# Optimization experiments

Hardware: AMD Instinct MI355X
Metric: run time of the kernel (lower is better)

## Reference

```python
import jax, jax.numpy as jnp
import numpy as np

HEADS = 16
DIM_HEAD = 64
SCALE = DIM_HEAD ** -0.5


def setup_inputs() -> dict:
    key = jax.random.key(0)
    k1, k2, k3 = jax.random.split(key, 3)
    B, N, C = 2, 2048, 1024
    inner = HEADS * DIM_HEAD  # 1024
    x = jax.random.normal(k1, (B, N, C), dtype=jnp.float32)
    w_qkv = jax.random.normal(k2, (C, 3 * inner), dtype=jnp.float32) * (C ** -0.5)
    w_proj = jax.random.normal(k3, (inner, C), dtype=jnp.float32) * (inner ** -0.5)
    b_proj = jnp.zeros((C,), dtype=jnp.float32)
    return {"x": x, "w_qkv": w_qkv, "w_proj": w_proj, "b_proj": b_proj}


def reference(x, w_qkv, w_proj, b_proj):
    B, N, C = x.shape
    qkv = x @ w_qkv  # [B, N, 3*inner]
    qkv = qkv.reshape(B, N, 3, HEADS, DIM_HEAD)
    qkv = jnp.transpose(qkv, (2, 0, 3, 1, 4))  # [3, B, H, N, D]
    q, k, v = qkv[0], qkv[1], qkv[2]
    q = q * SCALE
    attn = jnp.einsum('bhnd,bhmd->bhnm', q, k)  # [B, H, N, N]
    attn = jax.nn.softmax(attn, axis=-1)
    out = jnp.einsum('bhnm,bhmd->bhnd', attn, v)  # [B, H, N, D]
    out = jnp.transpose(out, (0, 2, 1, 3)).reshape(B, N, HEADS * DIM_HEAD)
    return out @ w_proj + b_proj
```

## Files before the change

### kernel.cpp

```cpp
#include <hip/hip_runtime.h>
#include <hip/hip_bf16.h>
#include <cstdint>
#include <cstddef>

static constexpr int BATCH = 2;
static constexpr int SEQ   = 2048;
static constexpr int CDIM  = 1024;
static constexpr int ROWS  = BATCH * SEQ;
static constexpr int QKVN  = 3 * CDIM;
static constexpr int QKN   = 2 * CDIM;

typedef short bf16x8 __attribute__((ext_vector_type(8)));
typedef short bf16x4 __attribute__((ext_vector_type(4)));
typedef float f32x4  __attribute__((ext_vector_type(4)));

__device__ inline short f2bf(float f) {
    union { float f; unsigned u; } v; v.f = f;
    unsigned u = v.u;
    u += 0x7fffu + ((u >> 16) & 1u);
    return (short)(u >> 16);
}

__device__ inline unsigned pk_bf16(float a, float b) {
#if __has_builtin(__builtin_amdgcn_cvt_pk_bf16_f32)
    auto r = __builtin_amdgcn_cvt_pk_bf16_f32(a, b);
    return __builtin_bit_cast(unsigned, r);
#else
    union { float f; unsigned u; } ua, ub;
    ua.f = a; ub.f = b;
    unsigned xa = ua.u + 0x7fffu + ((ua.u >> 16) & 1u);
    unsigned xb = ub.u + 0x7fffu + ((ub.u >> 16) & 1u);
    return __builtin_amdgcn_perm(xb, xa, 0x07060302);
#endif
}

__device__ inline void glds16(const short* g, short* l) {
    __builtin_amdgcn_global_load_lds(
        (const __attribute__((address_space(1))) void*)g,
        (__attribute__((address_space(3))) void*)l, 16, 0, 0);
}

__device__ inline f32x4 mfma16_bf16(bf16x4 a, bf16x4 b, f32x4 c) {
#if __has_builtin(__builtin_amdgcn_mfma_f32_16x16x16bf16_1k)
    return __builtin_amdgcn_mfma_f32_16x16x16bf16_1k(a, b, c, 0, 0, 0);
#else
    asm("v_mfma_f32_16x16x16_bf16 %0, %1, %2, %0" : "+v"(c) : "v"(a), "v"(b));
    return c;
#endif
}

__global__ __launch_bounds__(256) void prep(const float* __restrict__ x,
                                            const float* __restrict__ wqkv,
                                            const float* __restrict__ wproj,
                                            short* __restrict__ x_bf,
                                            short* __restrict__ wqkvT,
                                            short* __restrict__ wprojT,
                                            float smul) {
    __shared__ float tile[32][33];
    const int bid = blockIdx.x, t = threadIdx.x;
    if (bid < 4096) {
        int i = bid * 256 + t;
        float4 f = ((const float4*)x)[i];
        uint2 o;
        o.x = pk_bf16(f.x, f.y);
        o.y = pk_bf16(f.z, f.w);
        ((uint2*)x_bf)[i] = o;
        return;
    }
    const float* in; short* out; int C, r0, c0; float scale; int srows;
    if (bid < 7168) {
        int b2 = bid - 4096;
        in = wqkv; out = wqkvT; C = QKVN;
        c0 = (b2 % 96) * 32; r0 = (b2 / 96) * 32;
        scale = smul; srows = 1024;
    } else {
        int b3 = bid - 7168;
        in = wproj; out = wprojT; C = CDIM;
        c0 = (b3 & 31) * 32; r0 = (b3 >> 5) * 32;
        scale = 1.0f; srows = 0;
    }
    int tx = t & 31, ty = t >> 5;
    #pragma unroll
    for (int i = 0; i < 4; i++)
        tile[ty + i * 8][tx] = in[(size_t)(r0 + ty + i * 8) * C + c0 + tx];
    __syncthreads();
    #pragma unroll
    for (int i = 0; i < 4; i++) {
        int orow = c0 + ty + i * 8;
        float sc = (orow < srows) ? scale : 1.0f;
        out[(size_t)orow * CDIM + r0 + tx] = f2bf(tile[tx][ty + i * 8] * sc);
    }
}

template<int BF16OUT, int MT>
__device__ __forceinline__ void gemm_core(const short* __restrict__ A,
                                          const short* __restrict__ Bt,
                                          void* __restrict__ C,
                                          const float* __restrict__ bias,
                                          int N, int K, int m0, int n0,
                                          short* As, short* Bs) {
    constexpr int AF = MT / 32;
    const int t = threadIdx.x, wave = t >> 6, lane = t & 63;
    const int l15 = lane & 15, quad = lane >> 4;
    const int wr = wave >> 1, wc = wave & 1;

    f32x4 acc[AF][4] = {};

    const short* gA = A  + (size_t)(m0 + wave * (MT / 4) + (lane >> 2)) * K + (lane & 3) * 8;
    const short* gB = Bt + (size_t)(n0 + wave * 32 + (lane >> 2)) * K + (lane & 3) * 8;
    short* lA = &As[wave * (MT / 4) * 32];
    short* lB = &Bs[wave * 32 * 32];

    for (int k0 = 0; k0 < K; k0 += 32) {
        glds16(gA + k0, lA);
        if constexpr (MT == 128) glds16(gA + 16 * K + k0, lA + 512);
        glds16(gB + k0,          lB);
        glds16(gB + 16 * K + k0, lB + 512);
        __syncthreads();

        bf16x8 af[AF], bf[4];
        #pragma unroll
        for (int i = 0; i < AF; i++)
            af[i] = *(const bf16x8*)&As[(wr * (MT / 2) + i * 16 + l15) * 32 + quad * 8];
        #pragma unroll
        for (int j = 0; j < 4; j++)
            bf[j] = *(const bf16x8*)&Bs[(wc * 64 + j * 16 + l15) * 32 + quad * 8];
        #pragma unroll
        for (int i = 0; i < AF; i++)
            #pragma unroll
            for (int j = 0; j < 4; j++)
                acc[i][j] = __builtin_amdgcn_mfma_f32_16x16x32_bf16(af[i], bf[j], acc[i][j], 0, 0, 0);
        __syncthreads();
    }

    #pragma unroll
    for (int i = 0; i < AF; i++) {
        #pragma unroll
        for (int j = 0; j < 4; j++) {
            #pragma unroll
            for (int r = 0; r < 4; r++) {
                int row = m0 + wr * (MT / 2) + i * 16 + quad * 4 + r;
                int col = n0 + wc * 64 + j * 16 + l15;
                float v = acc[i][j][r];
                if (BF16OUT) ((short*)C)[(size_t)row * N + col] = f2bf(v);
                else         ((float*)C)[(size_t)row * N + col] = v + bias[col];
            }
        }
    }
}

__global__ __launch_bounds__(256) void gemm_qk_v(const short* __restrict__ x_bf,
                                                 const short* __restrict__ wqkvT,
                                                 short* __restrict__ qk,
                                                 short* __restrict__ vT) {
    __shared__ __align__(16) short As[128 * 32];
    __shared__ __align__(16) short Bs[128 * 32];
    const int bid = blockIdx.x;
    if (bid < 512) {
        gemm_core<1, 128>(x_bf, wqkvT, qk, nullptr, QKN, CDIM,
                          (bid >> 4) * 128, (bid & 15) * 128, As, Bs);
    } else {
        int b2 = bid - 512;
        gemm_core<1, 64>(wqkvT + (size_t)QKN * CDIM, x_bf, vT, nullptr, ROWS, CDIM,
                         (b2 >> 5) * 64, (b2 & 31) * 128, As, Bs);
    }
}

__global__ __launch_bounds__(256) void gemm_proj(const short* __restrict__ A,
                                                 const short* __restrict__ Bt,
                                                 float* __restrict__ C,
                                                 const float* __restrict__ bias) {
    __shared__ __align__(16) short As[64 * 32];
    __shared__ __align__(16) short Bs[128 * 32];
    gemm_core<0, 64>(A, Bt, C, bias, CDIM, CDIM,
                     blockIdx.y * 64, blockIdx.x * 128, As, Bs);
}

static constexpr int KP      = 128 * 32;
static constexpr int VT_OFF  = 2 * KP;
static constexpr int LDV     = 136;
static constexpr int SMEM_SH = VT_OFF + 64 * LDV;

__global__ __launch_bounds__(512) void attn_kernel(const short* __restrict__ qk,
                                                   const short* __restrict__ vTg,
                                                   short* __restrict__ attn_out) {
    __shared__ __align__(16) short smem[SMEM_SH];

    const int t = threadIdx.x, wave = t >> 6, lane = t & 63;
    const int l15 = lane & 15, quad = lane >> 4;
    const int bh = blockIdx.y, b = bh >> 4, h = bh & 15;
    const int q0 = blockIdx.x * 128;
    const size_t baseQ = (size_t)(b * SEQ) * QKN + h * 64;

    const size_t qoff = baseQ + (size_t)(q0 + wave * 16 + l15) * QKN + quad * 8;
    bf16x8 qf0 = *(const bf16x8*)&qk[qoff];
    bf16x8 qf1 = *(const bf16x8*)&qk[qoff + 32];

    const short* gK = qk + baseQ + 1024
                    + (size_t)(wave * 16 + (lane >> 2)) * QKN + (lane & 3) * 8;
    short* lK0 = smem + wave * 512;
    short* lK1 = smem + KP + wave * 512;

    const short* gV = vTg + (size_t)(h * 64) * ROWS + b * SEQ;
    const int vd = t >> 3, vc = t & 7;

    const bf16x4 ones = { (short)0x3F80, (short)0x3F80, (short)0x3F80, (short)0x3F80 };

    f32x4 ot[4] = {};
    f32x4 ol = {};

    for (int j0 = 0; j0 < SEQ; j0 += 128) {
        const size_t jadd = (size_t)j0 * QKN;
        glds16(gK + jadd,      lK0);
        glds16(gK + jadd + 32, lK1);
        {
            int4 v0 = *(const int4*)&gV[(size_t)vd * ROWS + j0 + vc * 8];
            int4 v1 = *(const int4*)&gV[(size_t)vd * ROWS + j0 + 64 + vc * 8];
            *(int4*)&smem[VT_OFF + vd * LDV + vc * 8]      = v0;
            *(int4*)&smem[VT_OFF + vd * LDV + 64 + vc * 8] = v1;
        }
        __syncthreads();

        #pragma unroll
        for (int sub = 0; sub < 8; sub++) {
            bf16x8 kf0 = *(const bf16x8*)&smem[(sub * 16 + l15) * 32 + quad * 8];
            bf16x8 kf1 = *(const bf16x8*)&smem[KP + (sub * 16 + l15) * 32 + quad * 8];
            f32x4 a = {};
            a = __builtin_amdgcn_mfma_f32_16x16x32_bf16(kf0, qf0, a, 0, 0, 0);
            a = __builtin_amdgcn_mfma_f32_16x16x32_bf16(kf1, qf1, a, 0, 0, 0);
            float p0 = __builtin_amdgcn_exp2f(a[0]);
            float p1 = __builtin_amdgcn_exp2f(a[1]);
            float p2 = __builtin_amdgcn_exp2f(a[2]);
            float p3 = __builtin_amdgcn_exp2f(a[3]);
            union { unsigned u[2]; bf16x4 v; } pu;
            pu.u[0] = pk_bf16(p0, p1);
            pu.u[1] = pk_bf16(p2, p3);
            ol = mfma16_bf16(ones, pu.v, ol);
            #pragma unroll
            for (int d = 0; d < 4; d++) {
                bf16x4 vf = *(const bf16x4*)&smem[VT_OFF + (d * 16 + l15) * LDV
                                                 + sub * 16 + quad * 4];
                ot[d] = mfma16_bf16(vf, pu.v, ot[d]);
            }
        }
        __syncthreads();
    }

    float inv = 1.0f / ol[0];
    #pragma unroll
    for (int d = 0; d < 4; d++) {
        unsigned w0 = pk_bf16(ot[d][0] * inv, ot[d][1] * inv);
        unsigned w1 = pk_bf16(ot[d][2] * inv, ot[d][3] * inv);
        *(unsigned*)&smem[(wave * 16 + l15) * 72 + d * 16 + quad * 4]     = w0;
        *(unsigned*)&smem[(wave * 16 + l15) * 72 + d * 16 + quad * 4 + 2] = w1;
    }
    __syncthreads();
    {
        int row = t >> 3, ch = t & 7;
        #pragma unroll
        for (int p = 0; p < 2; p++) {
            int rr = row + p * 64;
            int4 v = *(const int4*)&smem[rr * 72 + ch * 8];
            *(int4*)&attn_out[(size_t)(b * SEQ + q0 + rr) * CDIM + h * 64 + ch * 8] = v;
        }
    }
}

extern "C" void kernel_launch(void* const* d_in, const int* in_sizes, int n_in,
                              void* d_out, int out_size, void* d_ws, size_t ws_size,
                              hipStream_t stream) {
    const float* x      = (const float*)d_in[0];
    const float* w_qkv  = (const float*)d_in[1];
    const float* w_proj = (const float*)d_in[2];
    const float* b_proj = (const float*)d_in[3];
    float* out = (float*)d_out;

    char* ws = (char*)d_ws;
    short* x_bf    = (short*)(ws);
    short* wqkvT   = (short*)(ws + 8388608);
    short* wprojT  = (short*)(ws + 14680064);
    short* qk_bf   = (short*)(ws + 16777216);
    short* vTg     = (short*)(ws + 33554432);
    short* attn_bf = (short*)(ws + 41943040);

    const float SMUL = 0.125f * 1.44269504088896340736f;

    prep<<<8192, 256, 0, stream>>>(x, w_qkv, w_proj, x_bf, wqkvT, wprojT, SMUL);

    gemm_qk_v<<<1024, 256, 0, stream>>>(x_bf, wqkvT, qk_bf, vTg);

    attn_kernel<<<dim3(SEQ / 128, BATCH * 16), 512, 0, stream>>>(qk_bf, vTg, attn_bf);

    gemm_proj<<<dim3(CDIM / 128, ROWS / 64), 256, 0, stream>>>(attn_bf, wprojT, out, b_proj);
}
```

Before: 206.2 us.

## Double-buffer K and V tiles in attention kernel to overlap loads with MFMA

The attention loop now keeps two LDS buffers for the K and V^T tiles. It issues the global loads for the next 128-key tile before computing on the current one, which removes one barrier per iteration. The goal is to hide global memory latency behind the QK/PV MFMA work. In exchange, LDS use roughly doubles, which may reduce occupancy, and V values are held in registers across the compute loop, adding register pressure.

Result: faster. 200.9 us (-2.6%).

```diff
diff --git a/kernel.cpp b/kernel.cpp
--- a/kernel.cpp
+++ b/kernel.cpp
@@ -176,10 +176,11 @@
                      blockIdx.y * 64, blockIdx.x * 128, As, Bs);
 }
 
-static constexpr int KP      = 128 * 32;
-static constexpr int VT_OFF  = 2 * KP;
-static constexpr int LDV     = 136;
-static constexpr int SMEM_SH = VT_OFF + 64 * LDV;
+static constexpr int KBUF  = 2 * 128 * 32;
+static constexpr int VOFF  = 2 * KBUF;
+static constexpr int LDV   = 136;
+static constexpr int VBUF  = 64 * LDV;
+static constexpr int SMEM_SH = VOFF + 2 * VBUF;
 
 __global__ __launch_bounds__(512) void attn_kernel(const short* __restrict__ qk,
                                                    const short* __restrict__ vTg,
@@ -198,9 +199,6 @@
 
     const short* gK = qk + baseQ + 1024
                     + (size_t)(wave * 16 + (lane >> 2)) * QKN + (lane & 3) * 8;
-    short* lK0 = smem + wave * 512;
-    short* lK1 = smem + KP + wave * 512;
-
     const short* gV = vTg + (size_t)(h * 64) * ROWS + b * SEQ;
     const int vd = t >> 3, vc = t & 7;
 
@@ -209,22 +207,36 @@
     f32x4 ot[4] = {};
     f32x4 ol = {};
 
-    for (int j0 = 0; j0 < SEQ; j0 += 128) {
-        const size_t jadd = (size_t)j0 * QKN;
-        glds16(gK + jadd,      lK0);
-        glds16(gK + jadd + 32, lK1);
-        {
-            int4 v0 = *(const int4*)&gV[(size_t)vd * ROWS + j0 + vc * 8];
-            int4 v1 = *(const int4*)&gV[(size_t)vd * ROWS + j0 + 64 + vc * 8];
-            *(int4*)&smem[VT_OFF + vd * LDV + vc * 8]      = v0;
-            *(int4*)&smem[VT_OFF + vd * LDV + 64 + vc * 8] = v1;
-        }
+    glds16(gK,      smem + wave * 512);
+    glds16(gK + 32, smem + 4096 + wave * 512);
+    {
+        int4 va = *(const int4*)&gV[(size_t)vd * ROWS + vc * 8];
+        int4 vb = *(const int4*)&gV[(size_t)vd * ROWS + 64 + vc * 8];
+        *(int4*)&smem[VOFF + vd * LDV + vc * 8]      = va;
+        *(int4*)&smem[VOFF + vd * LDV + 64 + vc * 8] = vb;
+    }
+
+    for (int j = 0; j < SEQ / 128; j++) {
+        const int cur = j & 1, nxt = cur ^ 1;
         __syncthreads();
 
+        int4 va, vb;
+        if (j < SEQ / 128 - 1) {
+            const size_t jadd = (size_t)(j + 1) * 128 * QKN;
+            glds16(gK + jadd,      smem + nxt * KBUF + wave * 512);
+            glds16(gK + jadd + 32, smem + nxt * KBUF + 4096 + wave * 512);
+            va = *(const int4*)&gV[(size_t)vd * ROWS + (j + 1) * 128 + vc * 8];
+            vb = *(const int4*)&gV[(size_t)vd * ROWS + (j + 1) * 128 + 64 + vc * 8];
+        }
+
+        const short* Kb0 = smem + cur * KBUF;
+        const short* Kb1 = Kb0 + 4096;
+        const short* Vb  = smem + VOFF + cur * VBUF;
+
         #pragma unroll
         for (int sub = 0; sub < 8; sub++) {
-            bf16x8 kf0 = *(const bf16x8*)&smem[(sub * 16 + l15) * 32 + quad * 8];
-            bf16x8 kf1 = *(const bf16x8*)&smem[KP + (sub * 16 + l15) * 32 + quad * 8];
+            bf16x8 kf0 = *(const bf16x8*)&Kb0[(sub * 16 + l15) * 32 + quad * 8];
+            bf16x8 kf1 = *(const bf16x8*)&Kb1[(sub * 16 + l15) * 32 + quad * 8];
             f32x4 a = {};
             a = __builtin_amdgcn_mfma_f32_16x16x32_bf16(kf0, qf0, a, 0, 0, 0);
             a = __builtin_amdgcn_mfma_f32_16x16x32_bf16(kf1, qf1, a, 0, 0, 0);
@@ -238,12 +250,15 @@
             ol = mfma16_bf16(ones, pu.v, ol);
             #pragma unroll
             for (int d = 0; d < 4; d++) {
-                bf16x4 vf = *(const bf16x4*)&smem[VT_OFF + (d * 16 + l15) * LDV
-                                                 + sub * 16 + quad * 4];
+                bf16x4 vf = *(const bf16x4*)&Vb[(d * 16 + l15) * LDV + sub * 16 + quad * 4];
                 ot[d] = mfma16_bf16(vf, pu.v, ot[d]);
             }
         }
-        __syncthreads();
+
+        if (j < SEQ / 128 - 1) {
+            *(int4*)&smem[VOFF + nxt * VBUF + vd * LDV + vc * 8]      = va;
+            *(int4*)&smem[VOFF + nxt * VBUF + vd * LDV + 64 + vc * 8] = vb;
+        }
     }
 
     float inv = 1.0f / ol[0];
```
